# Performance work log

Measured on AMD Instinct MI355X. Metric: run time of the kernel, lower is better.

## Reference

```python
import jax, jax.numpy as jnp
import numpy as np
import math

EMBED = 1024
FF = 4096
HEADS = 16
HEAD = EMBED // HEADS
EPS = 1e-5


def new_gelu(x):
    c = math.sqrt(2.0 / math.pi)
    return 0.5 * x * (1.0 + jnp.tanh(c * (x + 0.044715 * x ** 3)))


def layer_norm(x, g, b):
    mu = jnp.mean(x, axis=-1, keepdims=True)
    var = jnp.var(x, axis=-1, keepdims=True)
    return (x - mu) * jax.lax.rsqrt(var + EPS) * g + b


def setup_inputs() -> dict:
    key = jax.random.key(0)
    ks = jax.random.split(key, 16)
    s = 0.02
    d = {
        'x': jax.random.normal(ks[0], (2, 2048, EMBED), jnp.float32),
        'Wq': jax.random.normal(ks[1], (EMBED, EMBED)) * s,
        'bq': jnp.zeros((EMBED,)),
        'Wk': jax.random.normal(ks[2], (EMBED, EMBED)) * s,
        'bk': jnp.zeros((EMBED,)),
        'Wv': jax.random.normal(ks[3], (EMBED, EMBED)) * s,
        'bv': jnp.zeros((EMBED,)),
        'Wp': jax.random.normal(ks[4], (EMBED, EMBED)) * s,
        'bp': jnp.zeros((EMBED,)),
        'W1': jax.random.normal(ks[5], (EMBED, FF)) * s,
        'b1': jnp.zeros((FF,)),
        'W2': jax.random.normal(ks[6], (FF, EMBED)) * s,
        'b2': jnp.zeros((EMBED,)),
        'g1': jnp.ones((EMBED,)), 'be1': jnp.zeros((EMBED,)),
        'g2': jnp.ones((EMBED,)), 'be2': jnp.zeros((EMBED,)),
    }
    return d


def reference(x, Wq, bq, Wk, bk, Wv, bv, Wp, bp, W1, b1, W2, b2, g1, be1, g2, be2):
    B, S, D = x.shape
    h = layer_norm(x, g1, be1)
    # project and split heads: [B,S,D] -> [B,H,S,Hd]
    def heads(y):
        return y.reshape(B, S, HEADS, HEAD).transpose(0, 2, 1, 3)
    Q = heads(h @ Wq + bq)
    K = heads(h @ Wk + bk)
    V = heads(h @ Wv + bv)
    att = jnp.einsum('bhqd,bhkd->bhqk', Q, K) / math.sqrt(HEAD)
    att = jax.nn.softmax(att, axis=-1)
    out = jnp.einsum('bhqk,bhkd->bhqd', att, V)
    out = out.transpose(0, 2, 1, 3).reshape(B, S, D)
    x = x + (out @ Wp + bp)  # dropout p=0 / eval -> identity
    h2 = layer_norm(x, g2, be2)
    x = x + (new_gelu(h2 @ W1 + b1) @ W2 + b2)
    return x
```

## Files before the change

### kernel.cpp

```cpp
#include <hip/hip_runtime.h>
#include <cstdint>


typedef __attribute__((ext_vector_type(8))) short short8;
typedef __attribute__((ext_vector_type(4))) float f32x4;

#define QSCL 0.18033688011112042f

__device__ __forceinline__ float bf2f(unsigned short u) {
    union { unsigned int i; float f; } v; v.i = ((unsigned int)u) << 16; return v.f;
}
__device__ __forceinline__ unsigned short f2bf(float f) {
    union { float f; unsigned int i; } v; v.f = f;
    unsigned int u = v.i;
    u += 0x7fff + ((u >> 16) & 1);
    return (unsigned short)(u >> 16);
}
__device__ __forceinline__ float gelu_f(float x) {
    float u = 0.7978845608028654f * (x + 0.044715f * x * x * x);
    float t = 1.f - 2.f / (__expf(2.f * u) + 1.f);
    return 0.5f * x * (1.f + t);
}
__device__ __forceinline__ void async16(const unsigned short* gp, unsigned short* lp) {
    __builtin_amdgcn_global_load_lds(
        (__attribute__((address_space(1))) void*)(gp),
        (__attribute__((address_space(3))) void*)(lp),
        16, 0, 0);
}

__device__ __forceinline__ void ln_dev(
    const float* __restrict__ x, const float* __restrict__ g,
    const float* __restrict__ b, unsigned short* __restrict__ o,
    int row, float* red)
{
    const int tid = threadIdx.x;
    const float4 v = ((const float4*)(x + (size_t)row * 1024))[tid];
    float f0 = v.x, f1 = v.y, f2 = v.z, f3 = v.w;
    float sum = f0 + f1 + f2 + f3;
    float sq  = f0 * f0 + f1 * f1 + f2 * f2 + f3 * f3;
    for (int off = 1; off < 64; off <<= 1) {
        sum += __shfl_xor(sum, off);
        sq  += __shfl_xor(sq,  off);
    }
    int wv = tid >> 6, ln = tid & 63;
    if (ln == 0) { red[wv] = sum; red[4 + wv] = sq; }
    __syncthreads();
    sum = red[0] + red[1] + red[2] + red[3];
    sq  = red[4] + red[5] + red[6] + red[7];
    float mu  = sum * (1.0f / 1024.0f);
    float var = sq  * (1.0f / 1024.0f) - mu * mu;
    float rsd = rsqrtf(fmaxf(var, 0.f) + 1e-5f);
    const float4 gg = ((const float4*)g)[tid];
    const float4 bb = ((const float4*)b)[tid];
    unsigned short* orow = o + (size_t)row * 1024;
    orow[4 * tid + 0] = f2bf((f0 - mu) * rsd * gg.x + bb.x);
    orow[4 * tid + 1] = f2bf((f1 - mu) * rsd * gg.y + bb.y);
    orow[4 * tid + 2] = f2bf((f2 - mu) * rsd * gg.z + bb.z);
    orow[4 * tid + 3] = f2bf((f3 - mu) * rsd * gg.w + bb.w);
}

__device__ __forceinline__ void transpose_dev(
    const float* __restrict__ in, unsigned short* __restrict__ out,
    int R, int C, int inStride, int bx, int by, unsigned short* tile ,
    float scale)
{
    const int tx = threadIdx.x & 15, ty = threadIdx.x >> 4;
    const int c0 = bx * 64, r0 = by * 64;
#pragma unroll
    for (int i = 0; i < 4; ++i) {
        int r = ty + 16 * i;
        float4 v = *(const float4*)(in + (size_t)(r0 + r) * inStride + c0 + tx * 4);
        tile[r * 70 + tx * 4 + 0] = f2bf(v.x * scale);
        tile[r * 70 + tx * 4 + 1] = f2bf(v.y * scale);
        tile[r * 70 + tx * 4 + 2] = f2bf(v.z * scale);
        tile[r * 70 + tx * 4 + 3] = f2bf(v.w * scale);
    }
    __syncthreads();
#pragma unroll
    for (int i = 0; i < 4; ++i) {
        int c = ty * 4 + i;
        ushort4 o;
        o.x = tile[(tx * 4 + 0) * 70 + c];
        o.y = tile[(tx * 4 + 1) * 70 + c];
        o.z = tile[(tx * 4 + 2) * 70 + c];
        o.w = tile[(tx * 4 + 3) * 70 + c];
        *(ushort4*)(out + (size_t)(c0 + c) * R + r0 + tx * 4) = o;
    }
}

__global__ __launch_bounds__(256) void ln_k(
    const float* __restrict__ x, const float* __restrict__ g,
    const float* __restrict__ b, unsigned short* __restrict__ o)
{
    __shared__ float red[8];
    ln_dev(x, g, b, o, blockIdx.x, red);
}
__global__ __launch_bounds__(256) void transpose_f2b(
    const float* __restrict__ in, unsigned short* __restrict__ out,
    int R, int C, int inStride, float scale)
{
    __shared__ unsigned short tile[64 * 70];
    transpose_dev(in, out, R, C, inStride, blockIdx.x, blockIdx.y, tile, scale);
}

__global__ __launch_bounds__(256) void prep1_k(
    const float* __restrict__ x,
    const float* __restrict__ g1, const float* __restrict__ be1,
    const float* __restrict__ Wq, const float* __restrict__ Wk,
    const float* __restrict__ Wv,
    const float* __restrict__ bq, const float* __restrict__ bk,
    const float* __restrict__ bv,
    unsigned short* __restrict__ hb,
    unsigned short* __restrict__ WTqkv,
    float* __restrict__ bcat)
{
    __shared__ unsigned short smem[64 * 70];
    const int b = blockIdx.x;
    if (b < 4096) {
        ln_dev(x, g1, be1, hb, b, (float*)smem);
    } else if (b < 4096 + 768) {
        int t = b - 4096;
        int w = t >> 8;
        int tt = t & 255;
        const float* W = (w == 0) ? Wq : (w == 1) ? Wk : Wv;
        transpose_dev(W, WTqkv + (size_t)w * 1024 * 1024,
                      1024, 1024, 1024, tt & 15, tt >> 4, smem,
                      (w == 0) ? QSCL : 1.f);
    } else {
        int i = (b - 4096 - 768) * 256 + threadIdx.x;
        float v = (i < 1024) ? bq[i] * QSCL : (i < 2048) ? bk[i - 1024] : bv[i - 2048];
        bcat[i] = v;
    }
}

__global__ __launch_bounds__(256) void prep2_k(
    const float* __restrict__ x1,
    const float* __restrict__ g2, const float* __restrict__ be2,
    const float* __restrict__ W1, const float* __restrict__ W2,
    unsigned short* __restrict__ h2,
    unsigned short* __restrict__ WT1,
    unsigned short* __restrict__ WT2)
{
    __shared__ unsigned short smem[64 * 70];
    const int b = blockIdx.x;
    if (b < 4096) {
        ln_dev(x1, g2, be2, h2, b, (float*)smem);
    } else if (b < 4096 + 1024) {
        int t = b - 4096;
        transpose_dev(W1, WT1, 1024, 4096, 4096, t & 63, t >> 6, smem, 1.f);
    } else {
        int t = b - 4096 - 1024;
        transpose_dev(W2, WT2, 4096, 1024, 1024, t & 15, t >> 4, smem, 1.f);
    }
}

__global__ __launch_bounds__(256) void vt_k(
    const unsigned short* __restrict__ src, int stride,
    unsigned short* __restrict__ Vt)
{
    __shared__ unsigned short tile[64][70];
    const int tx = threadIdx.x & 15, ty = threadIdx.x >> 4;
    const int t0 = blockIdx.x * 64;
    const int bh = blockIdx.y;
    const int bo = (bh >> 4) * 2048;
    const int ho = (bh & 15) * 64;
    const unsigned short* s = src + (size_t)bo * stride + ho;
#pragma unroll
    for (int i = 0; i < 4; ++i) {
        int r = ty + 16 * i;
        ushort4 v = *(const ushort4*)(s + (size_t)(t0 + r) * stride + tx * 4);
        tile[r][tx * 4 + 0] = v.x;
        tile[r][tx * 4 + 1] = v.y;
        tile[r][tx * 4 + 2] = v.z;
        tile[r][tx * 4 + 3] = v.w;
    }
    __syncthreads();
    unsigned short* dst = Vt + (size_t)bh * 64 * 2048;
    const int hh = tx >> 3;
    const int uu = (tx & 7) * 2;
#pragma unroll
    for (int i = 0; i < 4; ++i) {
        int d = ty * 4 + i;
        ushort4 o;
        o.x = tile[32 * hh + uu][d];
        o.y = tile[32 * hh + 16 + uu][d];
        o.z = tile[32 * hh + uu + 1][d];
        o.w = tile[32 * hh + 17 + uu][d];
        *(ushort4*)(dst + (size_t)d * 2048 + t0 + tx * 4) = o;
    }
}

__global__ __launch_bounds__(256, 3) void gemm_bt(
    const unsigned short* __restrict__ A,
    const unsigned short* __restrict__ Bt,
    const float* __restrict__ bias,
    const float* __restrict__ res,
    void* __restrict__ C,
    int M, int N, int K, int ldb, int dogelu, int out32, float bscale)
{
    __shared__ unsigned short sA[2 * 128 * 32];
    __shared__ unsigned short sB[2 * 128 * 32];
    const int tid  = threadIdx.x;
    const int wave = tid >> 6;
    const int lane = tid & 63;
    const int quad = lane >> 4;
    const int l15  = lane & 15;
    const int bm = blockIdx.y * 128;
    const int bn = blockIdx.x * 128;
    const int wM = (wave >> 1) * 64;
    const int wN = (wave & 1) * 64;

    f32x4 acc[4][4];
#pragma unroll
    for (int i = 0; i < 4; ++i)
#pragma unroll
        for (int j = 0; j < 4; ++j)
            acc[i][j] = (f32x4){0.f, 0.f, 0.f, 0.f};

    const int rowS = tid >> 2;
    const int kcS  = (tid & 3) * 8;
    const unsigned short* gA  = A  + (size_t)(bm + rowS) * K + kcS;
    const unsigned short* gA2 = gA + (size_t)64 * K;
    const unsigned short* gB  = Bt + (size_t)(bn + rowS) * ldb + kcS;
    const unsigned short* gB2 = gB + (size_t)64 * ldb;
    unsigned short* lA  = sA + tid * 8;
    unsigned short* lA2 = lA + 64 * 32;
    unsigned short* lB  = sB + tid * 8;
    unsigned short* lB2 = lB + 64 * 32;

    for (int k0 = 0; k0 < K; k0 += 64) {
        __syncthreads();
        async16(gA + k0,       lA);
        async16(gA2 + k0,      lA2);
        async16(gA + k0 + 32,  lA + 4096);
        async16(gA2 + k0 + 32, lA2 + 4096);
        async16(gB + k0,       lB);
        async16(gB2 + k0,      lB2);
        async16(gB + k0 + 32,  lB + 4096);
        async16(gB2 + k0 + 32, lB2 + 4096);
        __syncthreads();

#pragma unroll
        for (int p = 0; p < 2; ++p) {
            short8 aF[4], bF[4];
#pragma unroll
            for (int mi = 0; mi < 4; ++mi)
                aF[mi] = *(const short8*)(sA + p * 4096 + (wM + mi * 16 + l15) * 32 + quad * 8);
#pragma unroll
            for (int ni = 0; ni < 4; ++ni)
                bF[ni] = *(const short8*)(sB + p * 4096 + (wN + ni * 16 + l15) * 32 + quad * 8);
#pragma unroll
            for (int mi = 0; mi < 4; ++mi)
#pragma unroll
                for (int ni = 0; ni < 4; ++ni)
                    acc[mi][ni] = __builtin_amdgcn_mfma_f32_16x16x32_bf16(
                        aF[mi], bF[ni], acc[mi][ni], 0, 0, 0);
        }
    }

#pragma unroll
    for (int ni = 0; ni < 4; ++ni) {
        int col = bn + wN + ni * 16 + l15;
        float bv = bias ? bias[col] * bscale : 0.f;
#pragma unroll
        for (int mi = 0; mi < 4; ++mi) {
            int row = bm + wM + mi * 16 + quad * 4;
#pragma unroll
            for (int r = 0; r < 4; ++r) {
                float v = acc[mi][ni][r] + bv;
                if (dogelu) v = gelu_f(v);
                size_t idx = (size_t)(row + r) * N + col;
                if (res) v += res[idx];
                if (out32) ((float*)C)[idx] = v;
                else       ((unsigned short*)C)[idx] = f2bf(v);
            }
        }
    }
}

__global__ __launch_bounds__(256, 2) void gemm_bt64(
    const unsigned short* __restrict__ A,
    const unsigned short* __restrict__ Bt,
    const float* __restrict__ bias,
    const float* __restrict__ res,
    void* __restrict__ C,
    int M, int N, int K, int ldb, int dogelu, int out32)
{
    __shared__ unsigned short sA[2 * 128 * 32];
    __shared__ unsigned short sB[2 * 64 * 32];
    const int tid  = threadIdx.x;
    const int wave = tid >> 6;
    const int lane = tid & 63;
    const int quad = lane >> 4;
    const int l15  = lane & 15;
    const int bm = blockIdx.y * 128;
    const int bn = blockIdx.x * 64;
    const int wM = wave * 32;

    f32x4 acc[2][4];
#pragma unroll
    for (int i = 0; i < 2; ++i)
#pragma unroll
        for (int j = 0; j < 4; ++j)
            acc[i][j] = (f32x4){0.f, 0.f, 0.f, 0.f};

    const int rowS = tid >> 2;
    const int kcS  = (tid & 3) * 8;
    const unsigned short* gA  = A  + (size_t)(bm + rowS) * K + kcS;
    const unsigned short* gA2 = gA + (size_t)64 * K;
    const unsigned short* gB  = Bt + (size_t)(bn + rowS) * ldb + kcS;
    unsigned short* lA  = sA + tid * 8;
    unsigned short* lA2 = lA + 64 * 32;
    unsigned short* lB  = sB + tid * 8;

    for (int k0 = 0; k0 < K; k0 += 64) {
        __syncthreads();
        async16(gA + k0,       lA);
        async16(gA2 + k0,      lA2);
        async16(gA + k0 + 32,  lA + 4096);
        async16(gA2 + k0 + 32, lA2 + 4096);
        async16(gB + k0,       lB);
        async16(gB + k0 + 32,  lB + 2048);
        __syncthreads();

#pragma unroll
        for (int p = 0; p < 2; ++p) {
            short8 aF[2], bF[4];
#pragma unroll
            for (int mi = 0; mi < 2; ++mi)
                aF[mi] = *(const short8*)(sA + p * 4096 + (wM + mi * 16 + l15) * 32 + quad * 8);
#pragma unroll
            for (int ni = 0; ni < 4; ++ni)
                bF[ni] = *(const short8*)(sB + p * 2048 + (ni * 16 + l15) * 32 + quad * 8);
#pragma unroll
            for (int mi = 0; mi < 2; ++mi)
#pragma unroll
                for (int ni = 0; ni < 4; ++ni)
                    acc[mi][ni] = __builtin_amdgcn_mfma_f32_16x16x32_bf16(
                        aF[mi], bF[ni], acc[mi][ni], 0, 0, 0);
        }
    }

#pragma unroll
    for (int ni = 0; ni < 4; ++ni) {
        int col = bn + ni * 16 + l15;
        float bv = bias ? bias[col] : 0.f;
#pragma unroll
        for (int mi = 0; mi < 2; ++mi) {
            int row = bm + wM + mi * 16 + quad * 4;
#pragma unroll
            for (int r = 0; r < 4; ++r) {
                float v = acc[mi][ni][r] + bv;
                if (dogelu) v = gelu_f(v);
                size_t idx = (size_t)(row + r) * N + col;
                if (res) v += res[idx];
                if (out32) ((float*)C)[idx] = v;
                else       ((unsigned short*)C)[idx] = f2bf(v);
            }
        }
    }
}

__global__ __launch_bounds__(512, 1) void attn_k(
    const unsigned short* __restrict__ Q,
    const unsigned short* __restrict__ K,
    const unsigned short* __restrict__ Vt,
    unsigned short* __restrict__ O, int qs)
{
    __shared__ unsigned short smem[67584];
    unsigned short* sK = smem;
    unsigned short* sV = smem + 4 * 5632;
    unsigned short* sP = smem + 8 * 5632;

    const int tid  = threadIdx.x;
    const int wave = tid >> 6;
    const int g    = wave & 3;
    const int h    = wave >> 2;
    const int lane = tid & 63;
    const int quad = lane >> 4;
    const int l15  = lane & 15;
    const int bh = blockIdx.x * 4 + (blockIdx.y & 3);
    const int qb = (blockIdx.y >> 2) * 256;
    const int bo = (bh >> 4) * 2048;
    const int ho = (bh & 15) * 64;

    const unsigned short* Qb  = Q  + (size_t)bo * qs + ho;
    const unsigned short* Kb  = K  + (size_t)bo * qs + ho;
    const unsigned short* Vtb = Vt + (size_t)bh * 64 * 2048;
    unsigned short* sPg = sP + g * 5632;
    const int ni0 = 2 * h;

    short8 qF[2][4];
#pragma unroll
    for (int ks = 0; ks < 2; ++ks)
#pragma unroll
        for (int mi = 0; mi < 4; ++mi)
            qF[ks][mi] = *(const short8*)(Qb +
                (size_t)(qb + g * 64 + mi * 16 + l15) * qs + ks * 32 + quad * 8);

    short8 onesF;
#pragma unroll
    for (int j = 0; j < 8; ++j) onesF[j] = (short)0x3F80;

    f32x4 accO[4][4];
    f32x4 accL[4];
#pragma unroll
    for (int mi = 0; mi < 4; ++mi) {
        accL[mi] = (f32x4){0.f, 0.f, 0.f, 0.f};
#pragma unroll
        for (int nd = 0; nd < 4; ++nd) accO[mi][nd] = (f32x4){0.f, 0.f, 0.f, 0.f};
    }

    const int rowS = tid >> 3;
    const int dcS  = (tid & 7) * 8;

    short8 kr[2], vr[2];
#pragma unroll
    for (int s = 0; s < 2; ++s) {
        kr[s] = *(const short8*)(Kb + (size_t)(s * 64 + rowS) * qs + dcS);
        vr[s] = *(const short8*)(Vtb + (size_t)rowS * 2048 + s * 64 + dcS);
    }
#pragma unroll
    for (int s = 0; s < 2; ++s) {
        *(short8*)(sK + s * 5632 + rowS * 88 + dcS) = kr[s];
        *(short8*)(sV + s * 5632 + rowS * 88 + dcS) = vr[s];
    }
#pragma unroll
    for (int s = 0; s < 2; ++s) {
        kr[s] = *(const short8*)(Kb + (size_t)(128 + s * 64 + rowS) * qs + dcS);
        vr[s] = *(const short8*)(Vtb + (size_t)rowS * 2048 + 128 + s * 64 + dcS);
    }

    for (int kt = 0; kt < 2048; kt += 128) {
        const int buf = (kt >> 7) & 1;
        __syncthreads();

#pragma unroll
        for (int s = 0; s < 2; ++s) {
            const unsigned short* sKb = sK + (buf * 2 + s) * 5632;
            const unsigned short* sVb = sV + (buf * 2 + s) * 5632;

            short8 bK[2][2];
#pragma unroll
            for (int ks = 0; ks < 2; ++ks)
#pragma unroll
                for (int nj = 0; nj < 2; ++nj)
                    bK[ks][nj] = *(const short8*)(sKb +
                        ((ni0 + nj) * 16 + l15) * 88 + ks * 32 + quad * 8);

            f32x4 s0[4], s1[4];
#pragma unroll
            for (int mi = 0; mi < 4; ++mi) {
                s0[mi] = (f32x4){0.f, 0.f, 0.f, 0.f};
                s1[mi] = s0[mi];
#pragma unroll
                for (int ks = 0; ks < 2; ++ks) {
                    s0[mi] = __builtin_amdgcn_mfma_f32_16x16x32_bf16(qF[ks][mi], bK[ks][0], s0[mi], 0, 0, 0);
                    s1[mi] = __builtin_amdgcn_mfma_f32_16x16x32_bf16(qF[ks][mi], bK[ks][1], s1[mi], 0, 0, 0);
                }
            }

            if (s == 0 && kt + 128 < 2048) {
#pragma unroll
                for (int t = 0; t < 2; ++t) {
                    *(short8*)(sK + ((buf ^ 1) * 2 + t) * 5632 + rowS * 88 + dcS) = kr[t];
                    *(short8*)(sV + ((buf ^ 1) * 2 + t) * 5632 + rowS * 88 + dcS) = vr[t];
                }
                if (kt + 256 < 2048) {
#pragma unroll
                    for (int t = 0; t < 2; ++t) {
                        kr[t] = *(const short8*)(Kb + (size_t)(kt + 256 + t * 64 + rowS) * qs + dcS);
                        vr[t] = *(const short8*)(Vtb + (size_t)rowS * 2048 + kt + 256 + t * 64 + dcS);
                    }
                }
            }

#pragma unroll
            for (int mi = 0; mi < 4; ++mi)
#pragma unroll
                for (int r = 0; r < 4; ++r) {
                    float p0 = __builtin_amdgcn_exp2f(s0[mi][r]);
                    float p1 = __builtin_amdgcn_exp2f(s1[mi][r]);
                    unsigned int w;
                    asm("v_cvt_pk_bf16_f32 %0, %1, %2" : "=v"(w) : "v"(p0), "v"(p1));
                    *(unsigned int*)(sPg + (mi * 16 + quad * 4 + r) * 88 + h * 32 + l15 * 2) = w;
                }

            short8 aP[4], bV[4];
#pragma unroll
            for (int nd = 0; nd < 4; ++nd)
                bV[nd] = *(const short8*)(sVb + (nd * 16 + l15) * 88 + h * 32 + quad * 8);
#pragma unroll
            for (int mi = 0; mi < 4; ++mi)
                aP[mi] = *(const short8*)(sPg + (mi * 16 + l15) * 88 + h * 32 + quad * 8);

            __builtin_amdgcn_s_setprio(1);
#pragma unroll
            for (int mi = 0; mi < 4; ++mi) {
#pragma unroll
                for (int nd = 0; nd < 4; ++nd)
                    accO[mi][nd] = __builtin_amdgcn_mfma_f32_16x16x32_bf16(
                        aP[mi], bV[nd], accO[mi][nd], 0, 0, 0);
                accL[mi] = __builtin_amdgcn_mfma_f32_16x16x32_bf16(
                    aP[mi], onesF, accL[mi], 0, 0, 0);
            }
            __builtin_amdgcn_s_setprio(0);
        }
    }

    __syncthreads();
    float* scr = (float*)smem;
    float* po = scr + (size_t)(g * 64 + lane) * 68;
    float* pl = scr + 17408 + (size_t)(g * 64 + lane) * 20;
    if (h == 1) {
#pragma unroll
        for (int mi = 0; mi < 4; ++mi) {
#pragma unroll
            for (int nd = 0; nd < 4; ++nd)
                *(f32x4*)(po + mi * 16 + nd * 4) = accO[mi][nd];
            *(f32x4*)(pl + mi * 4) = accL[mi];
        }
    }
    __syncthreads();
    if (h == 0) {
#pragma unroll
        for (int mi = 0; mi < 4; ++mi) {
            accL[mi] += *(const f32x4*)(pl + mi * 4);
#pragma unroll
            for (int nd = 0; nd < 4; ++nd)
                accO[mi][nd] += *(const f32x4*)(po + mi * 16 + nd * 4);
        }
#pragma unroll
        for (int mi = 0; mi < 4; ++mi)
#pragma unroll
            for (int r = 0; r < 4; ++r) {
                int row = qb + g * 64 + mi * 16 + quad * 4 + r;
                float inv = 1.f / accL[mi][r];
#pragma unroll
                for (int nd = 0; nd < 4; ++nd)
                    O[(size_t)(bo + row) * 1024 + ho + nd * 16 + l15] =
                        f2bf(accO[mi][nd][r] * inv);
            }
    }
}

extern "C" void kernel_launch(void* const* d_in, const int* in_sizes, int n_in,
                              void* d_out, int out_size, void* d_ws, size_t ws_size,
                              hipStream_t stream)
{
    (void)in_sizes; (void)n_in; (void)out_size;
    const float* x   = (const float*)d_in[0];
    const float* Wq  = (const float*)d_in[1];
    const float* bq  = (const float*)d_in[2];
    const float* Wk  = (const float*)d_in[3];
    const float* bk  = (const float*)d_in[4];
    const float* Wv  = (const float*)d_in[5];
    const float* bv  = (const float*)d_in[6];
    const float* Wp  = (const float*)d_in[7];
    const float* bp  = (const float*)d_in[8];
    const float* W1  = (const float*)d_in[9];
    const float* b1  = (const float*)d_in[10];
    const float* W2  = (const float*)d_in[11];
    const float* b2  = (const float*)d_in[12];
    const float* g1  = (const float*)d_in[13];
    const float* be1 = (const float*)d_in[14];
    const float* g2  = (const float*)d_in[15];
    const float* be2 = (const float*)d_in[16];
    float* out = (float*)d_out;

    char* ws = (char*)d_ws;
    char* dob = (char*)d_out;
    const size_t MB = 1024 * 1024;

    if (ws_size >= 40 * MB) {
        unsigned short* hb    = (unsigned short*)dob;
        unsigned short* WTqkv = (unsigned short*)(dob + 8 * MB);
        float*          bcat  = (float*)(dob + 14 * MB);
        unsigned short* QKV   = (unsigned short*)ws;
        unsigned short* att   = (unsigned short*)(ws + 24 * MB);
        unsigned short* Vt    = (unsigned short*)(ws + 32 * MB);
        unsigned short* WTp   = (unsigned short*)(ws + 32 * MB);
        unsigned short* h2    = (unsigned short*)ws;
        unsigned short* WT1   = (unsigned short*)(ws + 8 * MB);
        unsigned short* WT2   = (unsigned short*)(ws + 16 * MB);
        unsigned short* act   = (unsigned short*)(ws + 24 * MB);

        prep1_k<<<4096 + 768 + 12, 256, 0, stream>>>(
            x, g1, be1, Wq, Wk, Wv, bq, bk, bv, hb, WTqkv, bcat);
        gemm_bt<<<dim3(24, 32), 256, 0, stream>>>(hb, WTqkv, bcat, nullptr, QKV,
                                                  4096, 3072, 1024, 1024, 0, 0, 1.f);
        vt_k<<<dim3(32, 32), 256, 0, stream>>>(QKV + 2048, 3072, Vt);
        attn_k<<<dim3(8, 32), 512, 0, stream>>>(QKV, QKV + 1024, Vt, att, 3072);
        transpose_f2b<<<dim3(16, 16), 256, 0, stream>>>(Wp, WTp, 1024, 1024, 1024, 1.f);
        gemm_bt64<<<dim3(16, 32), 256, 0, stream>>>(att, WTp, bp, x, out,
                                                    4096, 1024, 1024, 1024, 0, 1);
        prep2_k<<<4096 + 2048, 256, 0, stream>>>(out, g2, be2, W1, W2, h2, WT1, WT2);
        for (int c = 0; c < 2; ++c) {
            gemm_bt<<<dim3(16, 32), 256, 0, stream>>>(h2, WT1 + (size_t)c * 2048 * 1024,
                                                      b1 + c * 2048, nullptr, act,
                                                      4096, 2048, 1024, 1024, 1, 0, 1.f);
            gemm_bt64<<<dim3(16, 32), 256, 0, stream>>>(act, WT2 + (size_t)c * 2048,
                                                        c == 0 ? b2 : nullptr, out, out,
                                                        4096, 1024, 2048, 4096, 0, 1);
        }
    } else {
        unsigned short* Qw  = (unsigned short*)(ws);
        unsigned short* Kw  = (unsigned short*)(ws + 8 * MB);
        unsigned short* Vw  = (unsigned short*)(ws + 16 * MB);
        unsigned short* hb  = (unsigned short*)dob;
        unsigned short* WTq = (unsigned short*)(dob + 8 * MB);
        unsigned short* VtF = (unsigned short*)(dob + 8 * MB);
        unsigned short* att = Qw;
        unsigned short* WTb = Kw;
        unsigned short* h2  = Vw;
        unsigned short* act = Qw;

        ln_k<<<4096, 256, 0, stream>>>(x, g1, be1, hb);
        transpose_f2b<<<dim3(16, 16), 256, 0, stream>>>(Wq, WTq, 1024, 1024, 1024, QSCL);
        gemm_bt<<<dim3(8, 32), 256, 0, stream>>>(hb, WTq, bq, nullptr, Qw, 4096, 1024, 1024, 1024, 0, 0, QSCL);
        transpose_f2b<<<dim3(16, 16), 256, 0, stream>>>(Wk, WTq, 1024, 1024, 1024, 1.f);
        gemm_bt<<<dim3(8, 32), 256, 0, stream>>>(hb, WTq, bk, nullptr, Kw, 4096, 1024, 1024, 1024, 0, 0, 1.f);
        transpose_f2b<<<dim3(16, 16), 256, 0, stream>>>(Wv, WTq, 1024, 1024, 1024, 1.f);
        gemm_bt<<<dim3(8, 32), 256, 0, stream>>>(hb, WTq, bv, nullptr, Vw, 4096, 1024, 1024, 1024, 0, 0, 1.f);
        vt_k<<<dim3(32, 32), 256, 0, stream>>>(Vw, 1024, VtF);
        attn_k<<<dim3(8, 32), 512, 0, stream>>>(Qw, Kw, VtF, att, 1024);
        transpose_f2b<<<dim3(16, 16), 256, 0, stream>>>(Wp, WTb, 1024, 1024, 1024, 1.f);
        gemm_bt64<<<dim3(16, 32), 256, 0, stream>>>(att, WTb, bp, x, out, 4096, 1024, 1024, 1024, 0, 1);
        ln_k<<<4096, 256, 0, stream>>>(out, g2, be2, h2);
        for (int c = 0; c < 4; ++c) {
            transpose_f2b<<<dim3(16, 16), 256, 0, stream>>>(W1 + c * 1024, WTb, 1024, 1024, 4096, 1.f);
            gemm_bt64<<<dim3(16, 32), 256, 0, stream>>>(h2, WTb, b1 + c * 1024, nullptr, act,
                                                        4096, 1024, 1024, 1024, 1, 0);
            unsigned short* WT2c = WTb + 1024 * 1024;
            transpose_f2b<<<dim3(16, 16), 256, 0, stream>>>(W2 + (size_t)c * 1024 * 1024, WT2c,
                                                            1024, 1024, 1024, 1.f);
            gemm_bt64<<<dim3(16, 32), 256, 0, stream>>>(act, WT2c, c == 0 ? b2 : nullptr,
                                                        out, out, 4096, 1024, 1024, 1024, 0, 1);
        }
    }
}
```

Baseline: 378.4 us.

## Replace GEMM kernels with register-prefetched double-buffered 512-thread GEMM

Both GEMM kernels are replaced by one 512-thread, 128x128-tile kernel. It stages global tiles through registers into double-buffered, padded LDS (stride 68) instead of synchronous global-to-LDS loads, so the next tile's fetch overlaps with MFMA compute and the loop needs one barrier per K-step instead of two. Each wave computes a 64x32 subtile, and MFMA sections run at raised scheduling priority. The N=1024 GEMMs now use 128-wide tiles, which halves the number of blocks for those launches. Costs are higher register use, larger LDS per block (about 70KB), and fewer blocks on the narrower GEMMs.

```diff
diff --git a/kernel.cpp b/kernel.cpp
--- a/kernel.cpp
+++ b/kernel.cpp
@@ -20,12 +20,6 @@
     float u = 0.7978845608028654f * (x + 0.044715f * x * x * x);
     float t = 1.f - 2.f / (__expf(2.f * u) + 1.f);
     return 0.5f * x * (1.f + t);
-}
-__device__ __forceinline__ void async16(const unsigned short* gp, unsigned short* lp) {
-    __builtin_amdgcn_global_load_lds(
-        (__attribute__((address_space(1))) void*)(gp),
-        (__attribute__((address_space(3))) void*)(lp),
-        16, 0, 0);
 }
 
 __device__ __forceinline__ void ln_dev(
@@ -190,7 +184,7 @@
     }
 }
 
-__global__ __launch_bounds__(256, 3) void gemm_bt(
+__global__ __launch_bounds__(512, 4) void gemm5(
     const unsigned short* __restrict__ A,
     const unsigned short* __restrict__ Bt,
     const float* __restrict__ bias,
@@ -198,8 +192,8 @@
     void* __restrict__ C,
     int M, int N, int K, int ldb, int dogelu, int out32, float bscale)
 {
-    __shared__ unsigned short sA[2 * 128 * 32];
-    __shared__ unsigned short sB[2 * 128 * 32];
+    __shared__ unsigned short sA[2][128 * 68];
+    __shared__ unsigned short sB[2][128 * 68];
     const int tid  = threadIdx.x;
     const int wave = tid >> 6;
     const int lane = tid & 63;
@@ -207,146 +201,93 @@
     const int l15  = lane & 15;
     const int bm = blockIdx.y * 128;
     const int bn = blockIdx.x * 128;
-    const int wM = (wave >> 1) * 64;
-    const int wN = (wave & 1) * 64;
-
-    f32x4 acc[4][4];
+    const int wM = (wave & 1) * 64;
+    const int wN = (wave >> 1) * 32;
+
+    f32x4 acc[4][2];
 #pragma unroll
     for (int i = 0; i < 4; ++i)
 #pragma unroll
-        for (int j = 0; j < 4; ++j)
+        for (int j = 0; j < 2; ++j)
             acc[i][j] = (f32x4){0.f, 0.f, 0.f, 0.f};
 
-    const int rowS = tid >> 2;
-    const int kcS  = (tid & 3) * 8;
+    const int rowS = tid >> 3;
+    const int kcS  = (tid & 7) * 8;
     const unsigned short* gA  = A  + (size_t)(bm + rowS) * K + kcS;
     const unsigned short* gA2 = gA + (size_t)64 * K;
     const unsigned short* gB  = Bt + (size_t)(bn + rowS) * ldb + kcS;
     const unsigned short* gB2 = gB + (size_t)64 * ldb;
-    unsigned short* lA  = sA + tid * 8;
-    unsigned short* lA2 = lA + 64 * 32;
-    unsigned short* lB  = sB + tid * 8;
-    unsigned short* lB2 = lB + 64 * 32;
-
-    for (int k0 = 0; k0 < K; k0 += 64) {
+    const int lo1 = rowS * 68 + kcS;
+    const int lo2 = (rowS + 64) * 68 + kcS;
+
+    const int nt = K >> 6;
+    *(short8*)(&sA[0][lo1]) = *(const short8*)(gA);
+    *(short8*)(&sA[0][lo2]) = *(const short8*)(gA2);
+    *(short8*)(&sB[0][lo1]) = *(const short8*)(gB);
+    *(short8*)(&sB[0][lo2]) = *(const short8*)(gB2);
+    short8 ar1 = *(const short8*)(gA + 64);
+    short8 ar2 = *(const short8*)(gA2 + 64);
+    short8 br1 = *(const short8*)(gB + 64);
+    short8 br2 = *(const short8*)(gB2 + 64);
+
+    for (int t = 0; t < nt; ++t) {
+        const int buf = t & 1;
         __syncthreads();
-        async16(gA + k0,       lA);
-        async16(gA2 + k0,      lA2);
-        async16(gA + k0 + 32,  lA + 4096);
-        async16(gA2 + k0 + 32, lA2 + 4096);
-        async16(gB + k0,       lB);
-        async16(gB2 + k0,      lB2);
-        async16(gB + k0 + 32,  lB + 4096);
-        async16(gB2 + k0 + 32, lB2 + 4096);
-        __syncthreads();
-
-#pragma unroll
-        for (int p = 0; p < 2; ++p) {
-            short8 aF[4], bF[4];
-#pragma unroll
-            for (int mi = 0; mi < 4; ++mi)
-                aF[mi] = *(const short8*)(sA + p * 4096 + (wM + mi * 16 + l15) * 32 + quad * 8);
-#pragma unroll
-            for (int ni = 0; ni < 4; ++ni)
-                bF[ni] = *(const short8*)(sB + p * 4096 + (wN + ni * 16 + l15) * 32 + quad * 8);
-#pragma unroll
-            for (int mi = 0; mi < 4; ++mi)
-#pragma unroll
-                for (int ni = 0; ni < 4; ++ni)
-                    acc[mi][ni] = __builtin_amdgcn_mfma_f32_16x16x32_bf16(
-                        aF[mi], bF[ni], acc[mi][ni], 0, 0, 0);
-        }
-    }
-
-#pragma unroll
-    for (int ni = 0; ni < 4; ++ni) {
+
+        short8 aF[4], bF[2];
+#pragma unroll
+        for (int mi = 0; mi < 4; ++mi)
+            aF[mi] = *(const short8*)(&sA[buf][(wM + mi * 16 + l15) * 68 + quad * 8]);
+#pragma unroll
+        for (int ni = 0; ni < 2; ++ni)
+            bF[ni] = *(const short8*)(&sB[buf][(wN + ni * 16 + l15) * 68 + quad * 8]);
+
+        if (t + 1 < nt) {
+            *(short8*)(&sA[buf ^ 1][lo1]) = ar1;
+            *(short8*)(&sA[buf ^ 1][lo2]) = ar2;
+            *(short8*)(&sB[buf ^ 1][lo1]) = br1;
+            *(short8*)(&sB[buf ^ 1][lo2]) = br2;
+            if (t + 2 < nt) {
+                const int k2 = (t + 2) << 6;
+                ar1 = *(const short8*)(gA + k2);
+                ar2 = *(const short8*)(gA2 + k2);
+                br1 = *(const short8*)(gB + k2);
+                br2 = *(const short8*)(gB2 + k2);
+            }
+        }
+
+        __builtin_amdgcn_s_setprio(1);
+#pragma unroll
+        for (int mi = 0; mi < 4; ++mi)
+#pragma unroll
+            for (int ni = 0; ni < 2; ++ni)
+                acc[mi][ni] = __builtin_amdgcn_mfma_f32_16x16x32_bf16(
+                    aF[mi], bF[ni], acc[mi][ni], 0, 0, 0);
+        __builtin_amdgcn_s_setprio(0);
+
+#pragma unroll
+        for (int mi = 0; mi < 4; ++mi)
+            aF[mi] = *(const short8*)(&sA[buf][(wM + mi * 16 + l15) * 68 + 32 + quad * 8]);
+#pragma unroll
+        for (int ni = 0; ni < 2; ++ni)
+            bF[ni] = *(const short8*)(&sB[buf][(wN + ni * 16 + l15) * 68 + 32 + quad * 8]);
+
+        __builtin_amdgcn_s_setprio(1);
+#pragma unroll
+        for (int mi = 0; mi < 4; ++mi)
+#pragma unroll
+            for (int ni = 0; ni < 2; ++ni)
+                acc[mi][ni] = __builtin_amdgcn_mfma_f32_16x16x32_bf16(
+                    aF[mi], bF[ni], acc[mi][ni], 0, 0, 0);
+        __builtin_amdgcn_s_setprio(0);
+    }
+
+#pragma unroll
+    for (int ni = 0; ni < 2; ++ni) {
         int col = bn + wN + ni * 16 + l15;
         float bv = bias ? bias[col] * bscale : 0.f;
 #pragma unroll
         for (int mi = 0; mi < 4; ++mi) {
-            int row = bm + wM + mi * 16 + quad * 4;
-#pragma unroll
-            for (int r = 0; r < 4; ++r) {
-                float v = acc[mi][ni][r] + bv;
-                if (dogelu) v = gelu_f(v);
-                size_t idx = (size_t)(row + r) * N + col;
-                if (res) v += res[idx];
-                if (out32) ((float*)C)[idx] = v;
-                else       ((unsigned short*)C)[idx] = f2bf(v);
-            }
-        }
-    }
-}
-
-__global__ __launch_bounds__(256, 2) void gemm_bt64(
-    const unsigned short* __restrict__ A,
-    const unsigned short* __restrict__ Bt,
-    const float* __restrict__ bias,
-    const float* __restrict__ res,
-    void* __restrict__ C,
-    int M, int N, int K, int ldb, int dogelu, int out32)
-{
-    __shared__ unsigned short sA[2 * 128 * 32];
-    __shared__ unsigned short sB[2 * 64 * 32];
-    const int tid  = threadIdx.x;
-    const int wave = tid >> 6;
-    const int lane = tid & 63;
-    const int quad = lane >> 4;
-    const int l15  = lane & 15;
-    const int bm = blockIdx.y * 128;
-    const int bn = blockIdx.x * 64;
-    const int wM = wave * 32;
-
-    f32x4 acc[2][4];
-#pragma unroll
-    for (int i = 0; i < 2; ++i)
-#pragma unroll
-        for (int j = 0; j < 4; ++j)
-            acc[i][j] = (f32x4){0.f, 0.f, 0.f, 0.f};
-
-    const int rowS = tid >> 2;
-    const int kcS  = (tid & 3) * 8;
-    const unsigned short* gA  = A  + (size_t)(bm + rowS) * K + kcS;
-    const unsigned short* gA2 = gA + (size_t)64 * K;
-    const unsigned short* gB  = Bt + (size_t)(bn + rowS) * ldb + kcS;
-    unsigned short* lA  = sA + tid * 8;
-    unsigned short* lA2 = lA + 64 * 32;
-    unsigned short* lB  = sB + tid * 8;
-
-    for (int k0 = 0; k0 < K; k0 += 64) {
-        __syncthreads();
-        async16(gA + k0,       lA);
-        async16(gA2 + k0,      lA2);
-        async16(gA + k0 + 32,  lA + 4096);
-        async16(gA2 + k0 + 32, lA2 + 4096);
-        async16(gB + k0,       lB);
-        async16(gB + k0 + 32,  lB + 2048);
-        __syncthreads();
-
-#pragma unroll
-        for (int p = 0; p < 2; ++p) {
-            short8 aF[2], bF[4];
-#pragma unroll
-            for (int mi = 0; mi < 2; ++mi)
-                aF[mi] = *(const short8*)(sA + p * 4096 + (wM + mi * 16 + l15) * 32 + quad * 8);
-#pragma unroll
-            for (int ni = 0; ni < 4; ++ni)
-                bF[ni] = *(const short8*)(sB + p * 2048 + (ni * 16 + l15) * 32 + quad * 8);
-#pragma unroll
-            for (int mi = 0; mi < 2; ++mi)
-#pragma unroll
-                for (int ni = 0; ni < 4; ++ni)
-                    acc[mi][ni] = __builtin_amdgcn_mfma_f32_16x16x32_bf16(
-                        aF[mi], bF[ni], acc[mi][ni], 0, 0, 0);
-        }
-    }
-
-#pragma unroll
-    for (int ni = 0; ni < 4; ++ni) {
-        int col = bn + ni * 16 + l15;
-        float bv = bias ? bias[col] : 0.f;
-#pragma unroll
-        for (int mi = 0; mi < 2; ++mi) {
             int row = bm + wM + mi * 16 + quad * 4;
 #pragma unroll
             for (int r = 0; r < 4; ++r) {
@@ -462,15 +403,15 @@
 
             if (s == 0 && kt + 128 < 2048) {
 #pragma unroll
-                for (int t = 0; t < 2; ++t) {
-                    *(short8*)(sK + ((buf ^ 1) * 2 + t) * 5632 + rowS * 88 + dcS) = kr[t];
-                    *(short8*)(sV + ((buf ^ 1) * 2 + t) * 5632 + rowS * 88 + dcS) = vr[t];
+                for (int u = 0; u < 2; ++u) {
+                    *(short8*)(sK + ((buf ^ 1) * 2 + u) * 5632 + rowS * 88 + dcS) = kr[u];
+                    *(short8*)(sV + ((buf ^ 1) * 2 + u) * 5632 + rowS * 88 + dcS) = vr[u];
                 }
                 if (kt + 256 < 2048) {
 #pragma unroll
-                    for (int t = 0; t < 2; ++t) {
-                        kr[t] = *(const short8*)(Kb + (size_t)(kt + 256 + t * 64 + rowS) * qs + dcS);
-                        vr[t] = *(const short8*)(Vtb + (size_t)rowS * 2048 + kt + 256 + t * 64 + dcS);
+                    for (int u = 0; u < 2; ++u) {
+                        kr[u] = *(const short8*)(Kb + (size_t)(kt + 256 + u * 64 + rowS) * qs + dcS);
+                        vr[u] = *(const short8*)(Vtb + (size_t)rowS * 2048 + kt + 256 + u * 64 + dcS);
                     }
                 }
             }
@@ -587,21 +528,21 @@
 
         prep1_k<<<4096 + 768 + 12, 256, 0, stream>>>(
             x, g1, be1, Wq, Wk, Wv, bq, bk, bv, hb, WTqkv, bcat);
-        gemm_bt<<<dim3(24, 32), 256, 0, stream>>>(hb, WTqkv, bcat, nullptr, QKV,
-                                                  4096, 3072, 1024, 1024, 0, 0, 1.f);
+        gemm5<<<dim3(24, 32), 512, 0, stream>>>(hb, WTqkv, bcat, nullptr, QKV,
+                                                4096, 3072, 1024, 1024, 0, 0, 1.f);
         vt_k<<<dim3(32, 32), 256, 0, stream>>>(QKV + 2048, 3072, Vt);
         attn_k<<<dim3(8, 32), 512, 0, stream>>>(QKV, QKV + 1024, Vt, att, 3072);
         transpose_f2b<<<dim3(16, 16), 256, 0, stream>>>(Wp, WTp, 1024, 1024, 1024, 1.f);
-        gemm_bt64<<<dim3(16, 32), 256, 0, stream>>>(att, WTp, bp, x, out,
-                                                    4096, 1024, 1024, 1024, 0, 1);
+        gemm5<<<dim3(8, 32), 512, 0, stream>>>(att, WTp, bp, x, out,
+                                               4096, 1024, 1024, 1024, 0, 1, 1.f);
         prep2_k<<<4096 + 2048, 256, 0, stream>>>(out, g2, be2, W1, W2, h2, WT1, WT2);
         for (int c = 0; c < 2; ++c) {
-            gemm_bt<<<dim3(16, 32), 256, 0, stream>>>(h2, WT1 + (size_t)c * 2048 * 1024,
-                                                      b1 + c * 2048, nullptr, act,
-                                                      4096, 2048, 1024, 1024, 1, 0, 1.f);
-            gemm_bt64<<<dim3(16, 32), 256, 0, stream>>>(act, WT2 + (size_t)c * 2048,
-                                                        c == 0 ? b2 : nullptr, out, out,
-                                                        4096, 1024, 2048, 4096, 0, 1);
+            gemm5<<<dim3(16, 32), 512, 0, stream>>>(h2, WT1 + (size_t)c * 2048 * 1024,
+                                                    b1 + c * 2048, nullptr, act,
+                                                    4096, 2048, 1024, 1024, 1, 0, 1.f);
+            gemm5<<<dim3(8, 32), 512, 0, stream>>>(act, WT2 + (size_t)c * 2048,
+                                                   c == 0 ? b2 : nullptr, out, out,
+                                                   4096, 1024, 2048, 4096, 0, 1, 1.f);
         }
     } else {
         unsigned short* Qw  = (unsigned short*)(ws);
@@ -617,25 +558,25 @@
 
         ln_k<<<4096, 256, 0, stream>>>(x, g1, be1, hb);
         transpose_f2b<<<dim3(16, 16), 256, 0, stream>>>(Wq, WTq, 1024, 1024, 1024, QSCL);
-        gemm_bt<<<dim3(8, 32), 256, 0, stream>>>(hb, WTq, bq, nullptr, Qw, 4096, 1024, 1024, 1024, 0, 0, QSCL);
+        gemm5<<<dim3(8, 32), 512, 0, stream>>>(hb, WTq, bq, nullptr, Qw, 4096, 1024, 1024, 1024, 0, 0, QSCL);
         transpose_f2b<<<dim3(16, 16), 256, 0, stream>>>(Wk, WTq, 1024, 1024, 1024, 1.f);
-        gemm_bt<<<dim3(8, 32), 256, 0, stream>>>(hb, WTq, bk, nullptr, Kw, 4096, 1024, 1024, 1024, 0, 0, 1.f);
+        gemm5<<<dim3(8, 32), 512, 0, stream>>>(hb, WTq, bk, nullptr, Kw, 4096, 1024, 1024, 1024, 0, 0, 1.f);
         transpose_f2b<<<dim3(16, 16), 256, 0, stream>>>(Wv, WTq, 1024, 1024, 1024, 1.f);
-        gemm_bt<<<dim3(8, 32), 256, 0, stream>>>(hb, WTq, bv, nullptr, Vw, 4096, 1024, 1024, 1024, 0, 0, 1.f);
+        gemm5<<<dim3(8, 32), 512, 0, stream>>>(hb, WTq, bv, nullptr, Vw, 4096, 1024, 1024, 1024, 0, 0, 1.f);
         vt_k<<<dim3(32, 32), 256, 0, stream>>>(Vw, 1024, VtF);
         attn_k<<<dim3(8, 32), 512, 0, stream>>>(Qw, Kw, VtF, att, 1024);
         transpose_f2b<<<dim3(16, 16), 256, 0, stream>>>(Wp, WTb, 1024, 1024, 1024, 1.f);
-        gemm_bt64<<<dim3(16, 32), 256, 0, stream>>>(att, WTb, bp, x, out, 4096, 1024, 1024, 1024, 0, 1);
+        gemm5<<<dim3(8, 32), 512, 0, stream>>>(att, WTb, bp, x, out, 4096, 1024, 1024, 1024, 0, 1, 1.f);
         ln_k<<<4096, 256, 0, stream>>>(out, g2, be2, h2);
         for (int c = 0; c < 4; ++c) {
             transpose_f2b<<<dim3(16, 16), 256, 0, stream>>>(W1 + c * 1024, WTb, 1024, 1024, 4096, 1.f);
-            gemm_bt64<<<dim3(16, 32), 256, 0, stream>>>(h2, WTb, b1 + c * 1024, nullptr, act,
-                                                        4096, 1024, 1024, 1024, 1, 0);
+            gemm5<<<dim3(8, 32), 512, 0, stream>>>(h2, WTb, b1 + c * 1024, nullptr, act,
+                                                   4096, 1024, 1024, 1024, 1, 0, 1.f);
             unsigned short* WT2c = WTb + 1024 * 1024;
             transpose_f2b<<<dim3(16, 16), 256, 0, stream>>>(W2 + (size_t)c * 1024 * 1024, WT2c,
                                                             1024, 1024, 1024, 1.f);
-            gemm_bt64<<<dim3(16, 32), 256, 0, stream>>>(act, WT2c, c == 0 ? b2 : nullptr,
-                                                        out, out, 4096, 1024, 1024, 1024, 0, 1);
-        }
-    }
-}
+            gemm5<<<dim3(8, 32), 512, 0, stream>>>(act, WT2c, c == 0 ? b2 : nullptr,
+                                                   out, out, 4096, 1024, 1024, 1024, 0, 1, 1.f);
+        }
+    }
+}
```

Result: faster. 366.4 us (-3.2%).
